# Optimization experiments

Hardware: AMD Instinct MI355X
Metric: run time of the kernel (lower is better)

Reference implementation:

```python
import jax, jax.numpy as jnp
import numpy as np

NEG_INF = -9e15
ALPHA = 0.2  # LeakyReLU negative slope


def setup_inputs() -> dict:
    key = jax.random.key(0)
    k1, k2, k3, k4 = jax.random.split(key, 4)
    N, F_in, F_out = 8192, 128, 64
    h = jax.random.normal(k1, (N, F_in), dtype=jnp.float32)
    adj = jax.random.randint(k2, (N, N), 0, 2, dtype=jnp.int32)
    W = jax.random.normal(k3, (F_in, F_out), dtype=jnp.float32) * (1.414 / np.sqrt(F_in))
    a = jax.random.normal(k4, (2 * F_out, 1), dtype=jnp.float32) * 0.1
    return {"h": h, "adj": adj, "W": W, "a": a}


def reference(h, adj, W, a):
    # Wh: [N, F_out]
    Wh = h @ W
    F_out = Wh.shape[1]
    # Decomposed additive score: cat([Wh_i, Wh_j]) @ a == Wh_i@a1 + Wh_j@a2.
    # Identical math to the original repeat/cat/mm, without the [N*N, 2F] blowup.
    s1 = Wh @ a[:F_out, 0]   # [N] source-side score
    s2 = Wh @ a[F_out:, 0]   # [N] target-side score
    e = jax.nn.leaky_relu(s1[:, None] + s2[None, :], negative_slope=ALPHA)  # [N, N]
    attention = jax.nn.softmax(jnp.where(adj > 0, e, NEG_INF), axis=1)
    # dropout is identity in eval mode
    h_prime = attention @ Wh  # [N, F_out]
    return (h_prime, attention)
```

## Files before the change

### kernel.cpp

```cpp
#include <hip/hip_runtime.h>

#define NN 8192
#define FIN 128
#define FOUT 64
#define NEGINF (-9e15f)
#define LALPHA 0.2f

typedef float f32x4 __attribute__((ext_vector_type(4)));
typedef float f32x2 __attribute__((ext_vector_type(2)));
typedef short short8 __attribute__((ext_vector_type(8)));

__device__ __forceinline__ unsigned short f32_to_bf16(float x) {
  unsigned int u = __float_as_uint(x);
  u = (u + 0x7fffu + ((u >> 16) & 1u)) >> 16;
  return (unsigned short)u;
}
__device__ __forceinline__ float bf16_to_f32(unsigned short b) {
  return __uint_as_float(((unsigned int)b) << 16);
}

__global__ __launch_bounds__(256) void gat_prep(
    const float* __restrict__ h, const float* __restrict__ W,
    const float* __restrict__ a,
    float* __restrict__ s1g, float* __restrict__ s2g,
    unsigned short* __restrict__ whfh)
{
  __shared__ __align__(16) float Wl[FIN * FOUT];
  __shared__ __align__(16) float hl[16 * FIN];
  const int tid = threadIdx.x;
  const int i0 = blockIdx.x * 16;
  #pragma unroll
  for (int it = 0; it < 8; ++it) {
    int idx = (it * 256 + tid) * 4;
    *(f32x4*)&Wl[idx] = *(const f32x4*)&W[idx];
  }
  #pragma unroll
  for (int it = 0; it < 2; ++it) {
    int idx = (it * 256 + tid) * 4;
    *(f32x4*)&hl[idx] = *(const f32x4*)&h[(size_t)i0 * FIN + idx];
  }
  __syncthreads();
  const int r = tid >> 4;
  const int f0 = (tid & 15) * 4;
  f32x4 acc = {0.f, 0.f, 0.f, 0.f};
  #pragma unroll 8
  for (int k = 0; k < FIN; ++k) {
    float hv = hl[r * FIN + k];
    f32x4 wv = *(const f32x4*)&Wl[k * FOUT + f0];
    acc += hv * wv;
  }
  f32x4 a1v = *(const f32x4*)&a[f0];
  f32x4 a2v = *(const f32x4*)&a[FOUT + f0];
  float p1 = acc.x * a1v.x + acc.y * a1v.y + acc.z * a1v.z + acc.w * a1v.w;
  float p2 = acc.x * a2v.x + acc.y * a2v.y + acc.z * a2v.z + acc.w * a2v.w;
  #pragma unroll
  for (int d = 1; d < 16; d <<= 1) {
    p1 += __shfl_xor(p1, d, 16);
    p2 += __shfl_xor(p2, d, 16);
  }
  const int j = i0 + r;
  if ((tid & 15) == 0) { s1g[j] = p1; s2g[j] = p2; }
  const int kstep = j >> 5;
  const int lhi = (j >> 3) & 3;
  const int ein = j & 7;
  #pragma unroll
  for (int e = 0; e < 4; ++e) {
    int f = f0 + e;
    unsigned short hb = f32_to_bf16(acc[e]);
    int ln = lhi * 16 + (f & 15);
    whfh[(size_t)(kstep * 4 + (f >> 4)) * 512 + ln * 8 + ein] = hb;
  }
}

__global__ __launch_bounds__(256, 4) void gat_mask(
    const int* __restrict__ adj,
    const float* __restrict__ s1g, const float* __restrict__ s2g,
    float* __restrict__ outa,
    float* __restrict__ mrow, float* __restrict__ rlrow)
{
  __shared__ __align__(16) float s2l[NN];
  __shared__ unsigned long long mw[4][128];
  const int tid = threadIdx.x;
  const int lane = tid & 63;
  const int wv = tid >> 6;
  const int row = blockIdx.x * 4 + wv;
  #pragma unroll
  for (int it = 0; it < 8; ++it) {
    int idx = (it * 256 + tid) * 4;
    *(f32x4*)&s2l[idx] = *(const f32x4*)&s2g[idx];
  }
  __syncthreads();
  const int* __restrict__ ar = adj + (size_t)row * NN;
  float mx = -3.4e38f;
  #pragma unroll 4
  for (int it = 0; it < 128; ++it) {
    int jj = it * 64 + lane;
    int av = __builtin_nontemporal_load(&ar[jj]);
    unsigned long long b = __ballot(av > 0);
    mx = fmaxf(mx, (av > 0) ? s2l[jj] : -3.4e38f);
    if (lane == 0) mw[wv][it] = b;
  }
  #pragma unroll
  for (int d = 1; d < 64; d <<= 1) mx = fmaxf(mx, __shfl_xor(mx, d));
  const float s1v = s1g[row];
  const float z = s1v + mx;
  const float m = (mx <= -3.3e38f) ? NEGINF : fmaxf(z, LALPHA * z);
  float ls = 0.f;
  for (int it = 0; it < 128; ++it) {
    int jj = it * 64 + lane;
    unsigned long long b = mw[wv][it];
    float x = s1v + s2l[jj];
    x = fmaxf(x, LALPHA * x);
    x = ((b >> lane) & 1ull) ? x : NEGINF;
    ls += __expf(x - m);
  }
  #pragma unroll
  for (int d = 1; d < 64; d <<= 1) ls += __shfl_xor(ls, d);
  if (lane == 0) { mrow[row] = m; rlrow[row] = 1.f / ls; }
  unsigned long long* mrowg = (unsigned long long*)(outa + (size_t)row * NN);
  mrowg[lane] = mw[wv][lane];
  mrowg[lane + 64] = mw[wv][lane + 64];
}

__global__ __launch_bounds__(512, 4) void gat_attn(
    const float* __restrict__ s1g, const float* __restrict__ s2g,
    const float* __restrict__ mrow, const float* __restrict__ rlrow,
    const unsigned short* __restrict__ whfh,
    float* __restrict__ outh, float* __restrict__ outa)
{
  __shared__ __align__(16) float s2l[NN];
  __shared__ unsigned int maskl[16][258];
  __shared__ __align__(16) float red[4][1024];
  __shared__ float rowp[16][3];
  const int tid = threadIdx.x;
  const int lane = tid & 63;
  const int wv = tid >> 6;
  const int i0 = blockIdx.x * 16;

  #pragma unroll
  for (int it = 0; it < 4; ++it) {
    int idx = (it * 512 + tid) * 4;
    *(f32x4*)&s2l[idx] = *(const f32x4*)&s2g[idx];
  }
  #pragma unroll
  for (int i = 0; i < 8; ++i) {
    int idx = i * 512 + tid;
    int r = idx >> 8, w = idx & 255;
    maskl[r][w] = ((const unsigned int*)(outa + (size_t)(i0 + r) * NN))[w];
  }
  if (tid < 16) {
    rowp[tid][0] = s1g[i0 + tid];
    rowp[tid][1] = mrow[i0 + tid];
    rowp[tid][2] = rlrow[i0 + tid];
  }
  __syncthreads();

  const int row = lane & 15;
  const int kg = lane >> 4;
  const float s1r = rowp[row][0];
  const float mr = rowp[row][1];
  const float rir = rowp[row][2];
  const int kbase = wv * 1024;
  f32x4 acc0 = {0,0,0,0}, acc1 = {0,0,0,0}, acc2 = {0,0,0,0}, acc3 = {0,0,0,0};
  float* __restrict__ orow = outa + (size_t)(i0 + row) * NN;
  const short8* __restrict__ bfrag = (const short8*)whfh;
  for (int step = 0; step < 32; ++step) {
    const int k0 = kbase + step * 32;
    const int jb = k0 + kg * 8;
    f32x4 sa = *(const f32x4*)&s2l[jb];
    f32x4 sb = *(const f32x4*)&s2l[jb + 4];
    unsigned int bits = maskl[row][k0 >> 5] >> (kg * 8);
    float s2v[8] = {sa.x, sa.y, sa.z, sa.w, sb.x, sb.y, sb.z, sb.w};
    float af[8];
    short8 AH, AL;
    #pragma unroll
    for (int e = 0; e < 8; ++e) {
      float x = s1r + s2v[e];
      x = fmaxf(x, LALPHA * x);
      x = ((bits >> e) & 1u) ? x : NEGINF;
      float p = __expf(x - mr) * rir;
      af[e] = p;
      unsigned short hb = f32_to_bf16(p);
      AH[e] = (short)hb;
      AL[e] = (short)f32_to_bf16(p - bf16_to_f32(hb));
    }
    f32x4 st0 = {af[0], af[1], af[2], af[3]};
    f32x4 st1 = {af[4], af[5], af[6], af[7]};
    __builtin_nontemporal_store(st0, (f32x4*)&orow[jb]);
    __builtin_nontemporal_store(st1, (f32x4*)&orow[jb + 4]);
    size_t fb = (size_t)(k0 >> 5) * 256 + lane;
    short8 B0 = bfrag[fb];
    short8 B1 = bfrag[fb + 64];
    short8 B2 = bfrag[fb + 128];
    short8 B3 = bfrag[fb + 192];
    acc0 = __builtin_amdgcn_mfma_f32_16x16x32_bf16(AH, B0, acc0, 0, 0, 0);
    acc1 = __builtin_amdgcn_mfma_f32_16x16x32_bf16(AH, B1, acc1, 0, 0, 0);
    acc2 = __builtin_amdgcn_mfma_f32_16x16x32_bf16(AH, B2, acc2, 0, 0, 0);
    acc3 = __builtin_amdgcn_mfma_f32_16x16x32_bf16(AH, B3, acc3, 0, 0, 0);
    acc0 = __builtin_amdgcn_mfma_f32_16x16x32_bf16(AL, B0, acc0, 0, 0, 0);
    acc1 = __builtin_amdgcn_mfma_f32_16x16x32_bf16(AL, B1, acc1, 0, 0, 0);
    acc2 = __builtin_amdgcn_mfma_f32_16x16x32_bf16(AL, B2, acc2, 0, 0, 0);
    acc3 = __builtin_amdgcn_mfma_f32_16x16x32_bf16(AL, B3, acc3, 0, 0, 0);
  }
  const int c15 = lane & 15;
  f32x4 av[4] = {acc0, acc1, acc2, acc3};
  float* myred = &red[wv & 3][0];
  if (wv < 4) {
    #pragma unroll
    for (int nt = 0; nt < 4; ++nt)
      #pragma unroll
      for (int rg = 0; rg < 4; ++rg)
        myred[(kg * 4 + rg) * 64 + nt * 16 + c15] = av[nt][rg];
  }
  __syncthreads();
  if (wv >= 4) {
    #pragma unroll
    for (int nt = 0; nt < 4; ++nt)
      #pragma unroll
      for (int rg = 0; rg < 4; ++rg)
        myred[(kg * 4 + rg) * 64 + nt * 16 + c15] += av[nt][rg];
  }
  __syncthreads();
  {
    int base = tid * 2;
    f32x2 r0 = *(f32x2*)&red[0][base];
    f32x2 r1 = *(f32x2*)&red[1][base];
    f32x2 r2 = *(f32x2*)&red[2][base];
    f32x2 r3 = *(f32x2*)&red[3][base];
    f32x2 s = r0 + r1 + r2 + r3;
    *(f32x2*)&outh[(size_t)i0 * FOUT + base] = s;
  }
}

extern "C" void kernel_launch(void* const* d_in, const int* in_sizes, int n_in,
                              void* d_out, int out_size, void* d_ws, size_t ws_size,
                              hipStream_t stream) {
  const float* h = (const float*)d_in[0];
  const int* adj = (const int*)d_in[1];
  const float* W = (const float*)d_in[2];
  const float* a = (const float*)d_in[3];
  float* outh = (float*)d_out;
  float* outa = outh + (size_t)NN * FOUT;
  char* ws = (char*)d_ws;
  float* s1g = (float*)ws;
  float* s2g = s1g + NN;
  float* mrowv = s2g + NN;
  float* rlrowv = mrowv + NN;
  unsigned short* whfh = (unsigned short*)(ws + 128 * 1024);
  gat_prep<<<512, 256, 0, stream>>>(h, W, a, s1g, s2g, whfh);
  gat_mask<<<2048, 256, 0, stream>>>(adj, s1g, s2g, outa, mrowv, rlrowv);
  gat_attn<<<512, 512, 0, stream>>>(s1g, s2g, mrowv, rlrowv, whfh, outh, outa);
}
```

Baseline: 584.0 us.

## Fuse mask/softmax-stats pass into attention kernel using global s2 max shift

Merges the mask-building and softmax-normalizer kernel into the attention kernel. Each block reads adj for its 16 rows, builds the bitmask in shared memory and computes the row sums. The exact masked row max is replaced by a bound from the global max of s2, which removes one pass over adj and the mask round trip through the output buffer. This risks exp underflow when the bound is far above the true masked max, and rows with no edges would produce inf normalizers.

```diff
diff --git a/kernel.cpp b/kernel.cpp
--- a/kernel.cpp
+++ b/kernel.cpp
@@ -9,6 +9,7 @@
 typedef float f32x4 __attribute__((ext_vector_type(4)));
 typedef float f32x2 __attribute__((ext_vector_type(2)));
 typedef short short8 __attribute__((ext_vector_type(8)));
+typedef unsigned long long ull;
 
 __device__ __forceinline__ unsigned short f32_to_bf16(float x) {
   unsigned int u = __float_as_uint(x);
@@ -72,86 +73,81 @@
   }
 }
 
-__global__ __launch_bounds__(256, 4) void gat_mask(
+__global__ __launch_bounds__(512, 4) void gat_fused(
     const int* __restrict__ adj,
     const float* __restrict__ s1g, const float* __restrict__ s2g,
-    float* __restrict__ outa,
-    float* __restrict__ mrow, float* __restrict__ rlrow)
-{
-  __shared__ __align__(16) float s2l[NN];
-  __shared__ unsigned long long mw[4][128];
-  const int tid = threadIdx.x;
-  const int lane = tid & 63;
-  const int wv = tid >> 6;
-  const int row = blockIdx.x * 4 + wv;
-  #pragma unroll
-  for (int it = 0; it < 8; ++it) {
-    int idx = (it * 256 + tid) * 4;
-    *(f32x4*)&s2l[idx] = *(const f32x4*)&s2g[idx];
-  }
-  __syncthreads();
-  const int* __restrict__ ar = adj + (size_t)row * NN;
-  float mx = -3.4e38f;
-  #pragma unroll 4
-  for (int it = 0; it < 128; ++it) {
-    int jj = it * 64 + lane;
-    int av = __builtin_nontemporal_load(&ar[jj]);
-    unsigned long long b = __ballot(av > 0);
-    mx = fmaxf(mx, (av > 0) ? s2l[jj] : -3.4e38f);
-    if (lane == 0) mw[wv][it] = b;
-  }
-  #pragma unroll
-  for (int d = 1; d < 64; d <<= 1) mx = fmaxf(mx, __shfl_xor(mx, d));
-  const float s1v = s1g[row];
-  const float z = s1v + mx;
-  const float m = (mx <= -3.3e38f) ? NEGINF : fmaxf(z, LALPHA * z);
-  float ls = 0.f;
-  for (int it = 0; it < 128; ++it) {
-    int jj = it * 64 + lane;
-    unsigned long long b = mw[wv][it];
-    float x = s1v + s2l[jj];
-    x = fmaxf(x, LALPHA * x);
-    x = ((b >> lane) & 1ull) ? x : NEGINF;
-    ls += __expf(x - m);
-  }
-  #pragma unroll
-  for (int d = 1; d < 64; d <<= 1) ls += __shfl_xor(ls, d);
-  if (lane == 0) { mrow[row] = m; rlrow[row] = 1.f / ls; }
-  unsigned long long* mrowg = (unsigned long long*)(outa + (size_t)row * NN);
-  mrowg[lane] = mw[wv][lane];
-  mrowg[lane + 64] = mw[wv][lane + 64];
-}
-
-__global__ __launch_bounds__(512, 4) void gat_attn(
-    const float* __restrict__ s1g, const float* __restrict__ s2g,
-    const float* __restrict__ mrow, const float* __restrict__ rlrow,
     const unsigned short* __restrict__ whfh,
     float* __restrict__ outh, float* __restrict__ outa)
 {
   __shared__ __align__(16) float s2l[NN];
-  __shared__ unsigned int maskl[16][258];
+  __shared__ __align__(16) unsigned int maskl[16][258];
   __shared__ __align__(16) float red[4][1024];
   __shared__ float rowp[16][3];
+  __shared__ float smaxl;
   const int tid = threadIdx.x;
   const int lane = tid & 63;
   const int wv = tid >> 6;
   const int i0 = blockIdx.x * 16;
 
+  float lmax = -3.4e38f;
   #pragma unroll
   for (int it = 0; it < 4; ++it) {
     int idx = (it * 512 + tid) * 4;
-    *(f32x4*)&s2l[idx] = *(const f32x4*)&s2g[idx];
-  }
-  #pragma unroll
-  for (int i = 0; i < 8; ++i) {
-    int idx = i * 512 + tid;
-    int r = idx >> 8, w = idx & 255;
-    maskl[r][w] = ((const unsigned int*)(outa + (size_t)(i0 + r) * NN))[w];
-  }
-  if (tid < 16) {
-    rowp[tid][0] = s1g[i0 + tid];
-    rowp[tid][1] = mrow[i0 + tid];
-    rowp[tid][2] = rlrow[i0 + tid];
+    f32x4 v = *(const f32x4*)&s2g[idx];
+    *(f32x4*)&s2l[idx] = v;
+    lmax = fmaxf(fmaxf(fmaxf(lmax, v.x), fmaxf(v.y, v.z)), v.w);
+  }
+  #pragma unroll
+  for (int d = 1; d < 64; d <<= 1) lmax = fmaxf(lmax, __shfl_xor(lmax, d));
+  if (lane == 0) red[0][wv] = lmax;
+  __syncthreads();
+  if (tid == 0) {
+    float m = red[0][0];
+    #pragma unroll
+    for (int w = 1; w < 8; ++w) m = fmaxf(m, red[0][w]);
+    smaxl = m;
+  }
+  __syncthreads();
+  const float smax = smaxl;
+
+  {
+    const int r0 = wv * 2, r1 = r0 + 1;
+    const float s1a = s1g[i0 + r0];
+    const float s1b = s1g[i0 + r1];
+    const float za = s1a + smax, zb = s1b + smax;
+    const float Ma = fmaxf(za, LALPHA * za);
+    const float Mb = fmaxf(zb, LALPHA * zb);
+    const int* __restrict__ ara = adj + (size_t)(i0 + r0) * NN;
+    const int* __restrict__ arb = adj + (size_t)(i0 + r1) * NN;
+    float la = 0.f, lb = 0.f;
+    #pragma unroll 4
+    for (int it = 0; it < 128; ++it) {
+      int jj = it * 64 + lane;
+      int a0 = ara[jj];
+      int a1 = arb[jj];
+      float sv = s2l[jj];
+      ull b0 = __ballot(a0 > 0);
+      ull b1 = __ballot(a1 > 0);
+      float xa = s1a + sv; xa = fmaxf(xa, LALPHA * xa);
+      float xb = s1b + sv; xb = fmaxf(xb, LALPHA * xb);
+      float ea = __expf(xa - Ma);
+      float eb = __expf(xb - Mb);
+      la += (a0 > 0) ? ea : 0.f;
+      lb += (a1 > 0) ? eb : 0.f;
+      if (lane == 0) {
+        *(ull*)&maskl[r0][it * 2] = b0;
+        *(ull*)&maskl[r1][it * 2] = b1;
+      }
+    }
+    #pragma unroll
+    for (int d = 1; d < 64; d <<= 1) {
+      la += __shfl_xor(la, d);
+      lb += __shfl_xor(lb, d);
+    }
+    if (lane == 0) {
+      rowp[r0][0] = s1a; rowp[r0][1] = Ma; rowp[r0][2] = 1.f / la;
+      rowp[r1][0] = s1b; rowp[r1][1] = Mb; rowp[r1][2] = 1.f / lb;
+    }
   }
   __syncthreads();
 
@@ -205,6 +201,7 @@
   const int c15 = lane & 15;
   f32x4 av[4] = {acc0, acc1, acc2, acc3};
   float* myred = &red[wv & 3][0];
+  __syncthreads();
   if (wv < 4) {
     #pragma unroll
     for (int nt = 0; nt < 4; ++nt)
@@ -244,10 +241,7 @@
   char* ws = (char*)d_ws;
   float* s1g = (float*)ws;
   float* s2g = s1g + NN;
-  float* mrowv = s2g + NN;
-  float* rlrowv = mrowv + NN;
   unsigned short* whfh = (unsigned short*)(ws + 128 * 1024);
   gat_prep<<<512, 256, 0, stream>>>(h, W, a, s1g, s2g, whfh);
-  gat_mask<<<2048, 256, 0, stream>>>(adj, s1g, s2g, outa, mrowv, rlrowv);
-  gat_attn<<<512, 512, 0, stream>>>(s1g, s2g, mrowv, rlrowv, whfh, outh, outa);
-}
+  gat_fused<<<512, 512, 0, stream>>>(adj, s1g, s2g, whfh, outh, outa);
+}
```

Result: faster. 565.4 us (-3.2%).
